# Kernel optimization log

Hardware: AMD Instinct MI355X
Metric: run time of the kernel (lower is better)

## Reference

```python
import jax, jax.numpy as jnp
import numpy as np

B, C, T, Q = 4, 64, 128, 128   # batch, channels (emb_dim), frames, freq bins
K = 8                          # unfold kernel size (stride 1)
H = 128                        # SRU hidden size per direction
D_IN = C * K                   # SRU input size after unfold
L = Q - K + 1                  # unfolded sequence length
EPS = 1e-5


def setup_inputs() -> dict:
    key = jax.random.key(0)
    ks = jax.random.split(key, 6)
    s = 0.02
    return {
        "features": jax.random.normal(ks[0], (B, C, T, Q), jnp.float32),
        "ln_gamma": jnp.ones((C,), jnp.float32),
        "ln_beta": jnp.zeros((C,), jnp.float32),
        # SRU per-direction weights: W maps D_IN -> [x_tilde | f_gate | r_gate | highway], each H wide
        "w_fwd": jax.random.normal(ks[1], (D_IN, 4 * H), jnp.float32) * s,
        "b_fwd": jnp.zeros((2 * H,), jnp.float32),   # [b_f | b_r]
        "w_bwd": jax.random.normal(ks[2], (D_IN, 4 * H), jnp.float32) * s,
        "b_bwd": jnp.zeros((2 * H,), jnp.float32),
        # ConvTranspose1d weight in PyTorch layout [in_ch=2H, out_ch=C, K]
        "ct_w": jax.random.normal(ks[3], (2 * H, C, K), jnp.float32) * s,
        "ct_b": jnp.zeros((C,), jnp.float32),
    }


def _sru_dir(seq, W, b, reverse):
    """One SRU direction. seq: [N, L, D_IN] -> h: [N, L, H].
    c_t = f_t*c_{t-1} + (1-f_t)*x~_t ;  h_t = r_t*tanh(c_t) + (1-r_t)*x'_t
    (x' is the highway projection since input dim != hidden dim)."""
    U = seq @ W                                   # [N, L, 4H] -- dominant GEMM
    xt, f_pre, r_pre, xp = jnp.split(U, 4, axis=-1)
    bf, br = jnp.split(b, 2)
    f = jax.nn.sigmoid(f_pre + bf)
    r = jax.nn.sigmoid(r_pre + br)
    u = (1.0 - f) * xt
    if reverse:
        f = jnp.flip(f, 1)
        u = jnp.flip(u, 1)
    def combine(x, y):  # linear recurrence c = a*c_prev + b, y is the later element
        return (x[0] * y[0], x[1] * y[0] + y[1])
    c = jax.lax.associative_scan(combine, (f, u), axis=1)[1]
    if reverse:
        c = jnp.flip(c, 1)
    return r * jnp.tanh(c) + (1.0 - r) * xp


def reference(features, ln_gamma, ln_beta, w_fwd, b_fwd, w_bwd, b_bwd, ct_w, ct_b):
    # LayerNorm([C,1,1]): normalize over channel dim per (b,t,q)
    mu = jnp.mean(features, axis=1, keepdims=True)
    var = jnp.var(features, axis=1, keepdims=True)
    x = (features - mu) * jax.lax.rsqrt(var + EPS)
    x = x * ln_gamma[None, :, None, None] + ln_beta[None, :, None, None]

    N = B * T
    x = x.transpose(0, 2, 1, 3).reshape(N, C, Q)          # [B*T, C, Q]
    # nn.Unfold((K,1), stride 1): channel-major patch layout -> [N, C*K, L]
    u = jnp.stack([x[:, :, i:i + L] for i in range(K)], axis=2).reshape(N, C * K, L)
    seq = u.transpose(0, 2, 1)                            # [N, L, C*K]

    h = jnp.concatenate(
        [_sru_dir(seq, w_fwd, b_fwd, False), _sru_dir(seq, w_bwd, b_bwd, True)],
        axis=-1,
    )                                                      # [N, L, 2H]

    # ConvTranspose1d(2H -> C, K, stride=1) == full correlation with flipped kernel
    rhs = jnp.flip(ct_w, -1).transpose(1, 0, 2)           # [C, 2H, K]
    y = jax.lax.conv_general_dilated(
        h.transpose(0, 2, 1), rhs, (1,), [(K - 1, K - 1)],
        dimension_numbers=("NCH", "OIH", "NCH"),
    ) + ct_b[None, :, None]                               # [N, C, Q]

    y = y.reshape(B, T, C, Q).transpose(0, 2, 1, 3)       # [B, C, T, Q]
    return y + features
```

## Files before the change

### kernel.cpp

```cpp
#include <hip/hip_runtime.h>
#include <math.h>

#define BB 4
#define CC 64
#define TT 128
#define QQ 128
#define KK 8
#define HH 128
#define NN 512
#define LL 121
#define LPAD 135

typedef unsigned short ushort;
typedef __attribute__((ext_vector_type(8))) short short8;
typedef __attribute__((ext_vector_type(4))) float f32x4;
typedef __attribute__((ext_vector_type(4))) float float4v;

#define GLP(p) ((const __attribute__((address_space(1))) void*)(p))
#define LDP(p) ((__attribute__((address_space(3))) void*)(p))

__device__ __forceinline__ ushort f2bf(float x) {
  unsigned u = __float_as_uint(x);
  unsigned r = (u + 0x7FFFu + ((u >> 16) & 1u)) >> 16;
  return (ushort)r;
}

__global__ __launch_bounds__(256)
void prep_all(const float* __restrict__ f, const float* __restrict__ gamma,
              const float* __restrict__ beta, const float* __restrict__ wf,
              const float* __restrict__ wb, const float* __restrict__ ctw,
              ushort* __restrict__ xT, ushort* __restrict__ Bg,
              ushort* __restrict__ Bc2, ushort* __restrict__ zpage) {
  int bid = blockIdx.x, tid = threadIdx.x;
  if (bid < 256) {
    int p = bid * 256 + tid;
    int q = p & (QQ - 1);
    int t = (p >> 7) & (TT - 1);
    int b = p >> 14;
    const float* base = f + (size_t)b * CC * TT * QQ + (size_t)t * QQ + q;
    float v[64];
#pragma unroll
    for (int c = 0; c < 64; ++c) v[c] = base[(size_t)c * TT * QQ];
    float s = 0.f, s2 = 0.f;
#pragma unroll
    for (int c = 0; c < 64; ++c) { s += v[c]; s2 += v[c] * v[c]; }
    float mu = s * (1.f / CC);
    float var = s2 * (1.f / CC) - mu * mu;
    float rs = rsqrtf(var + 1e-5f);
    int n = b * TT + t;
    ushort* dst = xT + (size_t)n * (CC * QQ) + (size_t)q * CC;
#pragma unroll
    for (int v8 = 0; v8 < 8; ++v8) {
      short8 ov;
#pragma unroll
      for (int e = 0; e < 8; ++e) {
        int c = v8 * 8 + e;
        ov[e] = (short)f2bf((v[c] - mu) * rs * gamma[c] + beta[c]);
      }
      *(short8*)(dst + v8 * 8) = ov;
    }
  } else if (bid < 2816) {
    int idx = (bid - 256) * 256 + tid;
    if (idx < 524288) {
      int jblk = idx >> 13, r1 = idx & 8191;
      int ks = r1 >> 10, r2 = r1 & 1023;
      int s = r2 >> 9, r3 = r2 & 511;
      int lk = r3 >> 7, r4 = r3 & 127;
      int jr = r4 >> 3, e = r4 & 7;
      int j = jblk * 16 + jr;
      int c = s * 32 + lk * 8 + e;
      int dir = j >> 9, t = j & 511;
      int h = (t >> 7) * 32 + ((t >> 6) & 1) * 16 + (t & 15);
      int quad = (t >> 4) & 3;
      const float* w = dir ? wb : wf;
      Bg[idx] = f2bf(w[(size_t)(c * 8 + ks) * 512 + quad * 128 + h]);
    } else {
      int i2 = idx - 524288;
      int win = i2 >> 12, r1 = i2 & 4095;
      int s = r1 >> 11, r2 = r1 & 2047;
      int lk = r2 >> 9, r3 = r2 & 511;
      int c = r3 >> 3, e = r3 & 7;
      int jo = (s * 4 + lk) * 8 + e;
      int kk = win >> 2, jh = (win >> 1) & 1, sub = win & 1;
      int j2h = jh * 128 + sub * 64 + jo;
      Bc2[i2] = f2bf(ctw[(size_t)j2h * (CC * KK) + c * KK + kk]);
    }
  } else {
    if (tid < 128) ((unsigned*)zpage)[tid] = 0u;
  }
}

__global__ __launch_bounds__(256, 2)
void gemm_mfma(const ushort* __restrict__ xT, const ushort* __restrict__ Bg,
               const float* __restrict__ b_fwd, const float* __restrict__ b_bwd,
               ushort* __restrict__ hp, int n0) {
  __shared__ __align__(16) ushort Hs[144 * 64];

  int tid = threadIdx.x;
  int nl = blockIdx.y;
  int r0 = blockIdx.x * 256;
  int lane = tid & 63, w = tid >> 6;
  int lrow = lane & 15, lk = lane >> 4;
  f32x4 acc[8][4] = {};
  const ushort* xTn = xT + (size_t)(n0 + nl) * (CC * QQ);

#pragma unroll
  for (int i = 0; i < 4; ++i) {
    int p = i * 256 + tid;
    int row = p >> 3, s3 = p & 7;
    int key = ((row >> 3) ^ row) & 7;
    const ushort* g = xTn + (size_t)row * CC + (s3 ^ key) * 8;
    ushort* l = &Hs[(size_t)(i * 256 + (tid & 192)) * 8];
    __builtin_amdgcn_global_load_lds(GLP(g), LDP(l), 16, 0, 0);
  }
  if (tid < 128) {
    int p = 1024 + tid;
    int row = p >> 3, s3 = p & 7;
    int srow = row < 135 ? row : 134;
    int key = ((row >> 3) ^ row) & 7;
    const ushort* g = xTn + (size_t)srow * CC + (s3 ^ key) * 8;
    ushort* l = &Hs[(size_t)(1024 + (tid & 64)) * 8];
    __builtin_amdgcn_global_load_lds(GLP(g), LDP(l), 16, 0, 0);
  }
  __syncthreads();

  int RLb = ((lrow & 0x0C) << 3) | (lrow & 3);
  const ushort* Bw = Bg + ((size_t)(blockIdx.x * 16 + w * 4) * 8192)
                   + lk * 128 + lrow * 8;
#pragma unroll 1
  for (int ks = 0; ks < 8; ++ks) {
#pragma unroll
    for (int s = 0; s < 2; ++s) {
      short8 a[8], b[4];
#pragma unroll
      for (int nn = 0; nn < 4; ++nn)
        b[nn] = *(const short8*)&Bw[(size_t)nn * 8192 + ks * 1024 + s * 512];
#pragma unroll
      for (int m = 0; m < 8; ++m) {
        int R = RLb + m * 4 + ks;
        int key = ((R >> 3) ^ R) & 7;
        int slot = (s * 4 + lk) ^ key;
        a[m] = *(const short8*)&Hs[R * 64 + slot * 8];
      }
#pragma unroll
      for (int m = 0; m < 8; ++m)
#pragma unroll
        for (int nn = 0; nn < 4; ++nn)
          acc[m][nn] = __builtin_amdgcn_mfma_f32_16x16x32_bf16(
              a[m], b[nn], acc[m][nn], 0, 0, 0);
    }
  }

  int dirf = r0 >> 9;
  int hgroup = ((r0 & 511) >> 7) + (w >> 1);
  int h = hgroup * 32 + (w & 1) * 16 + lrow;
  const float* bias = dirf ? b_bwd : b_fwd;
  float bf = bias[h], br = bias[128 + h];

  float F = 1.f, U = 0.f;
  if (dirf == 0) {
#pragma unroll
    for (int m = 0; m < 8; ++m)
#pragma unroll
      for (int g = 0; g < 4; ++g) {
        int l = lk * 32 + m * 4 + g;
        float xt = acc[m][0][g], fp = acc[m][1][g];
        float fg = 1.f / (1.f + __expf(-(fp + bf)));
        float u = (1.f - fg) * xt;
        if (l > 120) { fg = 1.f; u = 0.f; }
        U = fg * U + u;
        F = fg * F;
        acc[m][0][g] = F; acc[m][1][g] = U;
      }
  } else {
#pragma unroll
    for (int m = 7; m >= 0; --m)
#pragma unroll
      for (int g = 3; g >= 0; --g) {
        int l = lk * 32 + m * 4 + g;
        float xt = acc[m][0][g], fp = acc[m][1][g];
        float fg = 1.f / (1.f + __expf(-(fp + bf)));
        float u = (1.f - fg) * xt;
        if (l > 120) { fg = 1.f; u = 0.f; }
        U = fg * U + u;
        F = fg * F;
        acc[m][0][g] = F; acc[m][1][g] = U;
      }
  }
  int e = dirf ? 3 - lk : lk;
  float lpU = 0.f;
#pragma unroll
  for (int j = 0; j < 4; ++j) {
    int jl = dirf ? 3 - j : j;
    float tF = __shfl(F, (jl << 4) + lrow);
    float tU = __shfl(U, (jl << 4) + lrow);
    if (j < e) lpU = tF * lpU + tU;
  }
  float cinit = lpU;
  ushort* hpn = hp + (size_t)nl * LPAD * 256;
  int colbase = dirf * 128 + hgroup * 32 + (w & 1) * 16;
#pragma unroll
  for (int m = 0; m < 8; ++m) {
#pragma unroll
    for (int g = 0; g < 4; ++g) {
      int l = lk * 32 + m * 4 + g;
      float c = acc[m][1][g] + acc[m][0][g] * cinit;
      float rp = acc[m][2][g];
      float rg = 1.f / (1.f + __expf(-(rp + br)));
      float e2 = __expf(2.f * c);
      float th = (e2 - 1.f) / (e2 + 1.f);
      float ho = rg * th + (1.f - rg) * acc[m][3][g];
      hpn[(size_t)(l + 7) * 256 + colbase + lrow] = f2bf(ho);
    }
  }
}

__global__ __launch_bounds__(256)
void conv_mfma(const ushort* __restrict__ hp, const ushort* __restrict__ Bc2,
               const ushort* __restrict__ zpage, const float* __restrict__ ctb,
               const float* __restrict__ feat, float* __restrict__ out, int n0) {
  __shared__ __align__(16) ushort Hs[144 * 128];
  int tid = threadIdx.x;
  int nl = blockIdx.x;
  int lane = tid & 63, w = tid >> 6;
  int wr0 = (w >> 1) * 64, wc0 = (w & 1) * 32;
  int lrow = lane & 15, lk = lane >> 4;
  f32x4 acc[4][2] = {};
  const ushort* hpn = hp + (size_t)nl * LPAD * 256;
  const ushort* Bcw = Bc2 + lk * 512 + (wc0 + lrow) * 8;

#pragma unroll 1
  for (int jh = 0; jh < 2; ++jh) {
    if (jh) __syncthreads();
#pragma unroll
    for (int r = 0; r < 9; ++r) {
      int p = r * 256 + tid;
      int row = p >> 4, ds = p & 15;
      int cs = (ds & 8) | ((ds & 7) ^ (row & 7));
      const ushort* g = ((unsigned)(row - 7) <= 120u)
          ? hpn + (size_t)row * 256 + jh * 128 + cs * 8
          : zpage;
      ushort* l = &Hs[(size_t)(r * 256 + (tid & 192)) * 8];
      __builtin_amdgcn_global_load_lds(GLP(g), LDP(l), 16, 0, 0);
    }
    __syncthreads();
#pragma unroll 1
    for (int t = 0; t < 16; ++t) {
      int kk = t >> 1, sub = t & 1;
      int win = kk * 4 + jh * 2 + sub;
#pragma unroll
      for (int s = 0; s < 2; ++s) {
        short8 a[4], b[2];
#pragma unroll
        for (int nn = 0; nn < 2; ++nn)
          b[nn] = *(const short8*)&Bcw[(size_t)(win * 8 + s * 4) * 512 + nn * 128];
#pragma unroll
        for (int m = 0; m < 4; ++m) {
          int row = wr0 + m * 16 + lrow + 7 - kk;
          int slot = (sub * 8) | ((s * 4 + lk) ^ (row & 7));
          a[m] = *(const short8*)&Hs[row * 128 + slot * 8];
        }
#pragma unroll
        for (int m = 0; m < 4; ++m)
#pragma unroll
          for (int nn = 0; nn < 2; ++nn)
            acc[m][nn] = __builtin_amdgcn_mfma_f32_16x16x32_bf16(
                a[m], b[nn], acc[m][nn], 0, 0, 0);
      }
    }
  }
  int n = n0 + nl;
  int b = n >> 7, t = n & 127;
#pragma unroll
  for (int m = 0; m < 4; ++m) {
    int q0 = wr0 + m * 16 + lk * 4;
#pragma unroll
    for (int nn = 0; nn < 2; ++nn) {
      int c = wc0 + nn * 16 + lrow;
      size_t idx = (size_t)b * (CC * TT * QQ) + (size_t)c * (TT * QQ)
                 + (size_t)t * QQ + q0;
      float4v fv = *(const float4v*)&feat[idx];
      float cb = ctb[c];
      float4v ov;
#pragma unroll
      for (int g = 0; g < 4; ++g) ov[g] = acc[m][nn][g] + cb + fv[g];
      *(float4v*)&out[idx] = ov;
    }
  }
}

extern "C" void kernel_launch(void* const* d_in, const int* in_sizes, int n_in,
                              void* d_out, int out_size, void* d_ws, size_t ws_size,
                              hipStream_t stream) {
  const float* feat  = (const float*)d_in[0];
  const float* gamma = (const float*)d_in[1];
  const float* beta  = (const float*)d_in[2];
  const float* w_fwd = (const float*)d_in[3];
  const float* b_fwd = (const float*)d_in[4];
  const float* w_bwd = (const float*)d_in[5];
  const float* b_bwd = (const float*)d_in[6];
  const float* ct_w  = (const float*)d_in[7];
  const float* ct_b  = (const float*)d_in[8];
  float* out = (float*)d_out;

  char* wsb = (char*)d_ws;
  ushort* xT  = (ushort*)wsb;
  ushort* Bg  = (ushort*)(wsb + 8389632);
  ushort* Bc2 = (ushort*)(wsb + 9438208);
  ushort* zpg = (ushort*)(wsb + 9700352);
  size_t persist = 9700864;
  size_t per_n = 69120u;
  int NC = 4;
  for (int cand = 512; cand >= 4; cand >>= 1) {
    if (persist + (size_t)cand * per_n <= ws_size) { NC = cand; break; }
  }
  ushort* hpc = (ushort*)(wsb + persist);

  prep_all<<<dim3(2817), dim3(256), 0, stream>>>(feat, gamma, beta, w_fwd,
                                                 w_bwd, ct_w, xT, Bg, Bc2, zpg);

  for (int n0 = 0; n0 < NN; n0 += NC) {
    gemm_mfma<<<dim3(4, NC), dim3(256), 0, stream>>>(xT, Bg, b_fwd, b_bwd,
                                                     hpc, n0);
    conv_mfma<<<dim3(NC), dim3(256), 0, stream>>>(hpc, Bc2, zpg, ct_b, feat,
                                                  out, n0);
  }
}
```

Baseline: 119.2 us.

## Split conv kernel across Q halves and raise MFMA priority in GEMM

The transposed-conv kernel now launches two blocks per sequence, each covering 64 output frequency bins. Each block loads all 256 hidden channels at once into LDS (72 rows), which removes the two-pass loop and its extra barrier and halves the per-wave accumulators. Launch bounds now request 4 blocks per CU. The GEMM kernel also wraps its MFMA burst in s_setprio to favour matrix issue over other waves. The split reloads the 7-row halo twice and reads the conv weights twice per sequence.

```diff
diff --git a/kernel.cpp b/kernel.cpp
--- a/kernel.cpp
+++ b/kernel.cpp
@@ -142,12 +142,14 @@
         int slot = (s * 4 + lk) ^ key;
         a[m] = *(const short8*)&Hs[R * 64 + slot * 8];
       }
+      __builtin_amdgcn_s_setprio(1);
 #pragma unroll
       for (int m = 0; m < 8; ++m)
 #pragma unroll
         for (int nn = 0; nn < 4; ++nn)
           acc[m][nn] = __builtin_amdgcn_mfma_f32_16x16x32_bf16(
               a[m], b[nn], acc[m][nn], 0, 0, 0);
+      __builtin_amdgcn_s_setprio(0);
     }
   }
 
@@ -215,70 +217,69 @@
   }
 }
 
-__global__ __launch_bounds__(256)
+__global__ __launch_bounds__(256, 4)
 void conv_mfma(const ushort* __restrict__ hp, const ushort* __restrict__ Bc2,
                const ushort* __restrict__ zpage, const float* __restrict__ ctb,
                const float* __restrict__ feat, float* __restrict__ out, int n0) {
-  __shared__ __align__(16) ushort Hs[144 * 128];
+  __shared__ __align__(16) ushort Hs[72 * 256];
   int tid = threadIdx.x;
-  int nl = blockIdx.x;
+  int qh = blockIdx.x;
+  int nl = blockIdx.y;
   int lane = tid & 63, w = tid >> 6;
-  int wr0 = (w >> 1) * 64, wc0 = (w & 1) * 32;
+  int wr0 = (w >> 1) * 32, wc0 = (w & 1) * 32;
   int lrow = lane & 15, lk = lane >> 4;
-  f32x4 acc[4][2] = {};
+  f32x4 acc[2][2] = {};
   const ushort* hpn = hp + (size_t)nl * LPAD * 256;
   const ushort* Bcw = Bc2 + lk * 512 + (wc0 + lrow) * 8;
-
+  int qbase = qh * 64;
+
+#pragma unroll
+  for (int r = 0; r < 9; ++r) {
+    int p = r * 256 + tid;
+    int row = p >> 5, ck = p & 31;
+    int cs = (ck & 24) | ((ck & 7) ^ (row & 7));
+    int grow = qbase + row;
+    const ushort* g = ((unsigned)(grow - 7) <= 120u)
+        ? hpn + (size_t)grow * 256 + cs * 8
+        : zpage;
+    ushort* l = &Hs[(size_t)(r * 256 + (tid & 192)) * 8];
+    __builtin_amdgcn_global_load_lds(GLP(g), LDP(l), 16, 0, 0);
+  }
+  __syncthreads();
 #pragma unroll 1
-  for (int jh = 0; jh < 2; ++jh) {
-    if (jh) __syncthreads();
-#pragma unroll
-    for (int r = 0; r < 9; ++r) {
-      int p = r * 256 + tid;
-      int row = p >> 4, ds = p & 15;
-      int cs = (ds & 8) | ((ds & 7) ^ (row & 7));
-      const ushort* g = ((unsigned)(row - 7) <= 120u)
-          ? hpn + (size_t)row * 256 + jh * 128 + cs * 8
-          : zpage;
-      ushort* l = &Hs[(size_t)(r * 256 + (tid & 192)) * 8];
-      __builtin_amdgcn_global_load_lds(GLP(g), LDP(l), 16, 0, 0);
-    }
-    __syncthreads();
-#pragma unroll 1
-    for (int t = 0; t < 16; ++t) {
-      int kk = t >> 1, sub = t & 1;
-      int win = kk * 4 + jh * 2 + sub;
-#pragma unroll
-      for (int s = 0; s < 2; ++s) {
-        short8 a[4], b[2];
+  for (int t = 0; t < 32; ++t) {
+    int kk = t >> 2;
+    int sh = (((t >> 1) & 1) << 4) | ((t & 1) << 3);
+#pragma unroll
+    for (int s = 0; s < 2; ++s) {
+      short8 a[2], b[2];
+#pragma unroll
+      for (int nn = 0; nn < 2; ++nn)
+        b[nn] = *(const short8*)&Bcw[(size_t)(t * 8 + s * 4) * 512 + nn * 128];
+#pragma unroll
+      for (int m = 0; m < 2; ++m) {
+        int row = wr0 + m * 16 + lrow + 7 - kk;
+        int slot = sh | ((s * 4 + lk) ^ (row & 7));
+        a[m] = *(const short8*)&Hs[row * 256 + slot * 8];
+      }
+#pragma unroll
+      for (int m = 0; m < 2; ++m)
 #pragma unroll
         for (int nn = 0; nn < 2; ++nn)
-          b[nn] = *(const short8*)&Bcw[(size_t)(win * 8 + s * 4) * 512 + nn * 128];
-#pragma unroll
-        for (int m = 0; m < 4; ++m) {
-          int row = wr0 + m * 16 + lrow + 7 - kk;
-          int slot = (sub * 8) | ((s * 4 + lk) ^ (row & 7));
-          a[m] = *(const short8*)&Hs[row * 128 + slot * 8];
-        }
-#pragma unroll
-        for (int m = 0; m < 4; ++m)
-#pragma unroll
-          for (int nn = 0; nn < 2; ++nn)
-            acc[m][nn] = __builtin_amdgcn_mfma_f32_16x16x32_bf16(
-                a[m], b[nn], acc[m][nn], 0, 0, 0);
-      }
+          acc[m][nn] = __builtin_amdgcn_mfma_f32_16x16x32_bf16(
+              a[m], b[nn], acc[m][nn], 0, 0, 0);
     }
   }
   int n = n0 + nl;
-  int b = n >> 7, t = n & 127;
-#pragma unroll
-  for (int m = 0; m < 4; ++m) {
-    int q0 = wr0 + m * 16 + lk * 4;
+  int b = n >> 7, tt = n & 127;
+#pragma unroll
+  for (int m = 0; m < 2; ++m) {
+    int q0 = qbase + wr0 + m * 16 + lk * 4;
 #pragma unroll
     for (int nn = 0; nn < 2; ++nn) {
       int c = wc0 + nn * 16 + lrow;
       size_t idx = (size_t)b * (CC * TT * QQ) + (size_t)c * (TT * QQ)
-                 + (size_t)t * QQ + q0;
+                 + (size_t)tt * QQ + q0;
       float4v fv = *(const float4v*)&feat[idx];
       float cb = ctb[c];
       float4v ov;
@@ -322,7 +323,7 @@
   for (int n0 = 0; n0 < NN; n0 += NC) {
     gemm_mfma<<<dim3(4, NC), dim3(256), 0, stream>>>(xT, Bg, b_fwd, b_bwd,
                                                      hpc, n0);
-    conv_mfma<<<dim3(NC), dim3(256), 0, stream>>>(hpc, Bc2, zpg, ct_b, feat,
-                                                  out, n0);
-  }
-}
+    conv_mfma<<<dim3(2, NC), dim3(256), 0, stream>>>(hpc, Bc2, zpg, ct_b, feat,
+                                                     out, n0);
+  }
+}
```

Measured after the change: 115.4 us, median of 2. 3.1% less time.
